# Kernel optimization log

Hardware: AMD Instinct MI355X
Metric: run time of the kernel (lower is better)

## Reference

```python
import jax, jax.numpy as jnp
import numpy as np
from jax import lax

B, S, E = 512, 128, 7
H = 1024
PRED_LEN = 96


def setup_inputs() -> dict:
    key = jax.random.key(0)
    ks = jax.random.split(key, 10)
    u = lambda k, shape: jax.random.uniform(k, shape, jnp.float32, -0.1, 0.1)
    return {
        "x": jax.random.normal(ks[0], (B, S, E), jnp.float32),
        "Wi0": u(ks[1], (4 * H, E)),
        "Wh0": u(ks[2], (4 * H, H)),
        "b0": u(ks[3], (4 * H,)),
        "Wi1": u(ks[4], (4 * H, H)),
        "Wh1": u(ks[5], (4 * H, H)),
        "b1": u(ks[6], (4 * H,)),
        "Wfc": u(ks[7], (PRED_LEN * E, H)),
        "bfc": u(ks[8], (PRED_LEN * E,)),
    }


def _lstm_layer(xs, Wi, Wh, b):
    # xs: [B, S, in] -> hs: [B, S, H]; gate order i, f, g, o
    batch = xs.shape[0]
    hidden = Wh.shape[1]
    # precompute input projections for all timesteps in one big GEMM
    x_proj = jnp.einsum("bsi,gi->bsg", xs, Wi) + b  # [B, S, 4H]

    def step(carry, xp_t):
        h, c = carry
        gates = xp_t + h @ Wh.T  # [B, 4H]
        i_t, f_t, g_t, o_t = jnp.split(gates, 4, axis=-1)
        i_t = jax.nn.sigmoid(i_t)
        f_t = jax.nn.sigmoid(f_t)
        g_t = jnp.tanh(g_t)
        o_t = jax.nn.sigmoid(o_t)
        c = f_t * c + i_t * g_t
        h = o_t * jnp.tanh(c)
        return (h, c), h

    h0 = jnp.zeros((batch, hidden), xs.dtype)
    c0 = jnp.zeros((batch, hidden), xs.dtype)
    (_, _), hs = lax.scan(step, (h0, c0), jnp.swapaxes(x_proj, 0, 1))
    return jnp.swapaxes(hs, 0, 1)  # [B, S, H]


def reference(x, Wi0, Wh0, b0, Wi1, Wh1, b1, Wfc, bfc):
    h1 = _lstm_layer(x, Wi0, Wh0, b0)
    h2 = _lstm_layer(h1, Wi1, Wh1, b1)
    last = h2[:, -1, :]  # [B, H]
    pred = last @ Wfc.T + bfc  # [B, PRED_LEN*E]
    return pred.reshape(x.shape[0], PRED_LEN, E)
```

## Files before the change

kernel.cpp:

```cpp
#include <hip/hip_runtime.h>
#include <hip/hip_bf16.h>


typedef __bf16 bf16x8 __attribute__((ext_vector_type(8)));
typedef float  f32x4  __attribute__((ext_vector_type(4)));

#define HSZ   (512 * 1024)

__device__ __forceinline__ float sigm_f(float x) {
    x = fminf(30.f, fmaxf(-30.f, x));
    return 1.0f / (1.0f + __expf(-x));
}
__device__ __forceinline__ float tanh_f(float x) {
    x = fminf(30.f, fmaxf(-30.f, x));
    float e = __expf(-2.0f * x);
    return (1.0f - e) / (1.0f + e);
}

__device__ __forceinline__ int perm_row(int np) {
    int g = (np >> 4) & 3;
    int j = ((np >> 6) << 4) | (np & 15);
    return g * 1024 + j;
}

__device__ __forceinline__ void spin_ge(const int* p, int target) {
    while (__hip_atomic_load(p, __ATOMIC_RELAXED, __HIP_MEMORY_SCOPE_AGENT) < target)
        __builtin_amdgcn_s_sleep(1);
}
__device__ __forceinline__ void signal_inc(int* p) {
    __hip_atomic_fetch_add(p, 1, __ATOMIC_RELAXED, __HIP_MEMORY_SCOPE_AGENT);
}
__device__ __forceinline__ void inv_l1() {
    asm volatile("buffer_inv" ::: "memory");
}
__device__ __forceinline__ void store_ea(unsigned* p, unsigned v) {
    __hip_atomic_store(p, v, __ATOMIC_RELAXED, __HIP_MEMORY_SCOPE_AGENT);
}


__global__ void prep_w0(const float* __restrict__ Wh0, __bf16* __restrict__ W0p) {
    int idx = blockIdx.x * 256 + threadIdx.x;
    int np = idx >> 8, k4 = (idx & 255) << 2;
    int r = perm_row(np);
    float4 v = *(const float4*)(Wh0 + r * 1024 + k4);
    __bf16* o = W0p + np * 1024 + k4;
    o[0] = (__bf16)v.x; o[1] = (__bf16)v.y; o[2] = (__bf16)v.z; o[3] = (__bf16)v.w;
}

__global__ void prep_w1(const float* __restrict__ Wi1, const float* __restrict__ Wh1,
                        __bf16* __restrict__ W1p) {
    int idx = blockIdx.x * 256 + threadIdx.x;
    int np = idx >> 9, k4 = (idx & 511) << 2;
    int r = perm_row(np);
    const float* s = (k4 < 1024) ? (Wi1 + r * 1024 + k4) : (Wh1 + r * 1024 + (k4 - 1024));
    float4 v = *(const float4*)s;
    __bf16* o = W1p + np * 2048 + k4;
    o[0] = (__bf16)v.x; o[1] = (__bf16)v.y; o[2] = (__bf16)v.z; o[3] = (__bf16)v.w;
}

__global__ void prep_wfc(const float* __restrict__ Wfc, __bf16* __restrict__ Wfcp) {
    int idx = blockIdx.x * 256 + threadIdx.x;
    int n = idx >> 8, k4 = (idx & 255) << 2;
    __bf16* o = Wfcp + n * 1024 + k4;
    if (n < 672) {
        float4 v = *(const float4*)(Wfc + n * 1024 + k4);
        o[0] = (__bf16)v.x; o[1] = (__bf16)v.y; o[2] = (__bf16)v.z; o[3] = (__bf16)v.w;
    } else {
        o[0] = (__bf16)0.f; o[1] = (__bf16)0.f; o[2] = (__bf16)0.f; o[3] = (__bf16)0.f;
    }
}

__global__ void prep_small(const float* __restrict__ Wi0, const float* __restrict__ b0,
                           const float* __restrict__ b1,
                           float* __restrict__ Wi0p, float* __restrict__ b1p) {
    int np = blockIdx.x * 256 + threadIdx.x;
    int r = perm_row(np);
    float* o = Wi0p + np * 8;
    #pragma unroll
    for (int q = 0; q < 7; ++q) o[q] = Wi0[r * 7 + q];
    o[7] = b0[r];
    b1p[np] = b1[r];
}


template <bool D0, bool D1>
__device__ __forceinline__ void floop(const __bf16* __restrict__ abase,
                                      const __bf16* __restrict__ w0row,
                                      const __bf16* __restrict__ w1row,
                                      int tid,
                                      char* AldsB, char* B0ldsB, char* B1ldsB,
                                      f32x4 (&acc0)[4], f32x4 (&acc1)[4]) {
    const int a_r = tid >> 3;
    const int a_c = (tid & 7) << 3;
    const int b_r = tid >> 2;
    const int b_c = (tid & 3) << 4;
    const int l  = tid & 63, w = tid >> 6;
    const int wm = w & 3,   wn = w >> 2;
    const int lj = l & 15,  lq = l >> 4;
    const int r7 = lj & 7;

    const __bf16* arw = abase + a_r * 1024 + a_c;

    const int awr  = a_r * 128 + (((tid & 7) ^ (a_r & 7)) << 4);
    const int bwr0 = b_r * 128 + (((((tid & 3) << 1) | 0) ^ (b_r & 7)) << 4);
    const int bwr1 = b_r * 128 + (((((tid & 3) << 1) | 1) ^ (b_r & 7)) << 4);
    const int rc0 = ((lq     ) ^ r7) << 4;
    const int rc1 = ((lq | 4 ) ^ r7) << 4;

    uint4 ra, rb00, rb01, rb10, rb11;
    auto ld = [&](int k0) {
        ra = *(const uint4*)(arw + k0);
        if (D0) {
            const __bf16* p = w0row + k0;
            rb00 = *(const uint4*)(p);
            rb01 = *(const uint4*)(p + 8);
        }
        if (D1) {
            const __bf16* p = w1row + k0;
            rb10 = *(const uint4*)(p);
            rb11 = *(const uint4*)(p + 8);
        }
    };
    auto wr = [&](int buf) {
        *(uint4*)(AldsB + buf * 8192 + awr) = ra;
        if (D0) {
            char* Bl = B0ldsB + buf * 16384;
            *(uint4*)(Bl + bwr0) = rb00;
            *(uint4*)(Bl + bwr1) = rb01;
        }
        if (D1) {
            char* Bl = B1ldsB + buf * 16384;
            *(uint4*)(Bl + bwr0) = rb10;
            *(uint4*)(Bl + bwr1) = rb11;
        }
    };

    ld(0);
    wr(0);
    ld(64);
    __syncthreads();

    const char* Ap  = AldsB  + (wm * 16 + lj) * 128;
    const char* B0p = B0ldsB + (wn * 64 + lj) * 128;
    const char* B1p = B1ldsB + (wn * 64 + lj) * 128;

    for (int it = 0; it < 16; ++it) {
        const int bo = it & 1;
        const char* Ab  = Ap  + bo * 8192;
        const char* B0b = B0p + bo * 16384;
        const char* B1b = B1p + bo * 16384;
        #pragma unroll
        for (int s = 0; s < 2; ++s) {
            const int rc = s ? rc1 : rc0;
            bf16x8 af = *(const bf16x8*)(Ab + rc);
            #pragma unroll
            for (int ni = 0; ni < 4; ++ni) {
                if (D0) {
                    bf16x8 b0 = *(const bf16x8*)(B0b + ni * 2048 + rc);
                    acc0[ni] = __builtin_amdgcn_mfma_f32_16x16x32_bf16(af, b0, acc0[ni], 0, 0, 0);
                }
                if (D1) {
                    bf16x8 b1 = *(const bf16x8*)(B1b + ni * 2048 + rc);
                    acc1[ni] = __builtin_amdgcn_mfma_f32_16x16x32_bf16(af, b1, acc1[ni], 0, 0, 0);
                }
            }
        }
        if (it + 1 < 16) wr((it + 1) & 1);
        if (it + 2 < 16) ld((it + 2) * 64);
        __syncthreads();
    }
}


__global__ __launch_bounds__(512)
void lstm_persist(const float* __restrict__ x,
                  const __bf16* __restrict__ W0p, const __bf16* __restrict__ W1p,
                  const __bf16* __restrict__ Wfcp,
                  const float* __restrict__ Wi0p, const float* __restrict__ b1p,
                  const float* __restrict__ bfc,
                  __bf16* __restrict__ bufA, __bf16* __restrict__ bufB,
                  char* __restrict__ flagpage, float* __restrict__ out) {
    __shared__ __attribute__((aligned(16))) char Alds[2 * 8192];
    __shared__ __attribute__((aligned(16))) char B0lds[2 * 16384];
    __shared__ __attribute__((aligned(16))) char B1lds[2 * 16384];
    __shared__ float Aux1[128];
    __shared__ float Xlds[64 * 9];
    __shared__ float Wxlds[128 * 9];
    __shared__ int role[2];

    const int tid = threadIdx.x;

    if (tid == 0) {
        int xcd = __builtin_amdgcn_s_getreg(63508) & 7;
        int* xcnt = (int*)(flagpage + 1024) + xcd;
        int slot = __hip_atomic_fetch_add(xcnt, 1, __ATOMIC_RELAXED,
                                          __HIP_MEMORY_SCOPE_AGENT);
        role[0] = xcd; role[1] = slot;
    }
    __syncthreads();
    const int xcd = role[0];
    const int sl  = role[1];
    const int mt = sl >> 2, nb = sl & 3;
    const int m0 = mt * 64;
    const int n0 = xcd * 512 + nb * 128;
    int* cnt = (int*)(flagpage + (size_t)mt * 64);

    if (tid < 128) {
        Aux1[tid] = b1p[n0 + tid];
    } else if (tid < 256) {
        int nl = tid - 128;
        const float* sp = Wi0p + (n0 + nl) * 8;
        float* d = Wxlds + nl * 9;
        #pragma unroll
        for (int q = 0; q < 8; ++q) d[q] = sp[q];
    }

    const int b_r = tid >> 2;
    const int b_c = (tid & 3) << 4;
    const int l  = tid & 63, w = tid >> 6;
    const int wm = w & 3,   wn = w >> 2;
    const int lj = l & 15,  lq = l >> 4;
    const int jc = (n0 >> 2) + wn * 16 + lj;

    const __bf16* w0row = W0p + (size_t)(n0 + b_r) * 1024 + b_c;
    const __bf16* w1row = W1p + (size_t)(n0 + b_r) * 2048 + b_c;

    float c0[4], c1[4];
    #pragma unroll
    for (int r = 0; r < 4; ++r) { c0[r] = 0.f; c1[r] = 0.f; }

    f32x4 acc0[4], acc1[4];

    for (int r = 0; r <= 128; ++r) {
        const bool do0 = (r < 128), do1 = (r > 0);
        const __bf16* haPrev = bufA + (size_t)(r % 3) * HSZ;
        __bf16*       haOut  = bufA + (size_t)((r + 1) % 3) * HSZ;
        const __bf16* hbPrev = bufB + (size_t)((r + 2) % 3) * HSZ;
        __bf16*       hbOut  = bufB + (size_t)(r % 3) * HSZ;

        if (tid == 0) spin_ge(cnt, 32 * r);
        __syncthreads();
        inv_l1();

        if (do0 && tid < 64) {
            const float* xr = x + (m0 + tid) * 896 + r * 7;
            float* d = Xlds + tid * 9;
            #pragma unroll
            for (int q = 0; q < 7; ++q) d[q] = xr[q];
            d[7] = 1.0f;
        }

        #pragma unroll
        for (int j = 0; j < 4; ++j) {
            acc0[j] = (f32x4){0.f, 0.f, 0.f, 0.f};
            acc1[j] = (f32x4){0.f, 0.f, 0.f, 0.f};
        }

        const __bf16* abase = haPrev + m0 * 1024;
        if (do0 && do1)
            floop<true, true >(abase, w0row, w1row, tid, Alds, B0lds, B1lds, acc0, acc1);
        else if (do0)
            floop<true, false>(abase, w0row, w1row, tid, Alds, B0lds, B1lds, acc0, acc1);
        else
            floop<false, true>(abase, w0row, w1row, tid, Alds, B0lds, B1lds, acc0, acc1);

        if (do1) {
            floop<false, true>(hbPrev + m0 * 1024, w0row, w1row + 1024,
                               tid, Alds, B0lds, B1lds, acc0, acc1);
        }

        if (do0) {
            #pragma unroll
            for (int rr = 0; rr < 4; ++rr) {
                int ml = wm * 16 + lq * 4 + rr;
                int m  = m0 + ml;
                float pre[4];
                #pragma unroll
                for (int g = 0; g < 4; ++g) pre[g] = acc0[g][rr];
                const float* xr = Xlds + ml * 9;
                #pragma unroll
                for (int g = 0; g < 4; ++g) {
                    const float* wx = Wxlds + (wn * 64 + g * 16 + lj) * 9;
                    float sv = 0.f;
                    #pragma unroll
                    for (int q = 0; q < 8; ++q) sv += xr[q] * wx[q];
                    pre[g] += sv;
                }
                float ig = sigm_f(pre[0]);
                float fg = sigm_f(pre[1]);
                float gv = tanh_f(pre[2]);
                float og = sigm_f(pre[3]);
                float cn = fg * c0[rr] + ig * gv;
                c0[rr] = cn;
                float hv = og * tanh_f(cn);
                unsigned u32 = __builtin_bit_cast(unsigned, hv);
                unsigned hu = (u32 + 0x7fffu + ((u32 >> 16) & 1u)) >> 16;
                int pv = __shfl_xor((int)hu, 1, 64);
                if ((lj & 1) == 0)
                    store_ea((unsigned*)(haOut + (size_t)m * 1024 + jc),
                             hu | ((unsigned)pv << 16));
            }
        }
        if (do1) {
            #pragma unroll
            for (int rr = 0; rr < 4; ++rr) {
                int m = m0 + wm * 16 + lq * 4 + rr;
                float pre[4];
                #pragma unroll
                for (int g = 0; g < 4; ++g)
                    pre[g] = acc1[g][rr] + Aux1[wn * 64 + g * 16 + lj];
                float ig = sigm_f(pre[0]);
                float fg = sigm_f(pre[1]);
                float gv = tanh_f(pre[2]);
                float og = sigm_f(pre[3]);
                float cn = fg * c1[rr] + ig * gv;
                c1[rr] = cn;
                float hv = og * tanh_f(cn);
                unsigned u32 = __builtin_bit_cast(unsigned, hv);
                unsigned hu = (u32 + 0x7fffu + ((u32 >> 16) & 1u)) >> 16;
                int pv = __shfl_xor((int)hu, 1, 64);
                if ((lj & 1) == 0)
                    store_ea((unsigned*)(hbOut + (size_t)m * 1024 + jc),
                             hu | ((unsigned)pv << 16));
            }
        }
        __syncthreads();
        if (tid == 0) signal_inc(cnt);
    }

    if (nb == 0 && xcd < 6) {
        const int n0fc = xcd * 128;
        if (tid == 0) spin_ge(cnt, 32 * 129);
        __syncthreads();
        inv_l1();
        if (tid < 128) {
            int n = n0fc + tid;
            Aux1[tid] = (n < 672) ? bfc[n] : 0.f;
        }
        #pragma unroll
        for (int j = 0; j < 4; ++j)
            acc0[j] = (f32x4){0.f, 0.f, 0.f, 0.f};
        floop<true, false>(bufB + (size_t)2 * HSZ + m0 * 1024,
                           Wfcp + (size_t)(n0fc + b_r) * 1024 + b_c, nullptr,
                           tid, Alds, B0lds, B1lds, acc0, acc1);
        #pragma unroll
        for (int rr = 0; rr < 4; ++rr) {
            int m = m0 + wm * 16 + lq * 4 + rr;
            #pragma unroll
            for (int ni = 0; ni < 4; ++ni) {
                int n = n0fc + wn * 64 + ni * 16 + lj;
                if (n < 672)
                    out[m * 672 + n] = acc0[ni][rr] + Aux1[wn * 64 + ni * 16 + lj];
            }
        }
    }
}

#define O_W0P   0u
#define O_W1P   8388608u
#define O_WFCP  25165824u
#define O_WI0P  26738688u
#define O_B1P   26869760u
#define O_FLG   26886144u
#define O_BA    26888192u
#define O_BB    30033920u
#define WS_NEED 33179648u

extern "C" void kernel_launch(void* const* d_in, const int* in_sizes, int n_in,
                              void* d_out, int out_size, void* d_ws, size_t ws_size,
                              hipStream_t stream) {
    const float* x   = (const float*)d_in[0];
    const float* Wi0 = (const float*)d_in[1];
    const float* Wh0 = (const float*)d_in[2];
    const float* b0  = (const float*)d_in[3];
    const float* Wi1 = (const float*)d_in[4];
    const float* Wh1 = (const float*)d_in[5];
    const float* b1  = (const float*)d_in[6];
    const float* Wfc = (const float*)d_in[7];
    const float* bfc = (const float*)d_in[8];
    float* out = (float*)d_out;
    char*  ws  = (char*)d_ws;
    if (ws_size < WS_NEED) return;

    __bf16* W0p  = (__bf16*)(ws + O_W0P);
    __bf16* W1p  = (__bf16*)(ws + O_W1P);
    __bf16* Wfcp = (__bf16*)(ws + O_WFCP);
    float*  Wi0p = (float*)(ws + O_WI0P);
    float*  b1p  = (float*)(ws + O_B1P);
    char*   flg  = (char*)(ws + O_FLG);
    __bf16* bufA = (__bf16*)(ws + O_BA);
    __bf16* bufB = (__bf16*)(ws + O_BB);

    hipMemsetAsync(ws + O_FLG, 0, 2048u + 1048576u, stream);
    hipMemsetAsync(ws + O_BB, 0, 1048576u, stream);

    prep_w0   <<<4096, 256, 0, stream>>>(Wh0, W0p);
    prep_w1   <<<8192, 256, 0, stream>>>(Wi1, Wh1, W1p);
    prep_wfc  <<<768,  256, 0, stream>>>(Wfc, Wfcp);
    prep_small<<<16,   256, 0, stream>>>(Wi0, b0, b1, Wi0p, b1p);

    lstm_persist<<<256, 512, 0, stream>>>(x, W0p, W1p, Wfcp, Wi0p, b1p, bfc,
                                          bufA, bufB, flg, out);
}
```

Before: 2.925 ms.

## Retile recurrent GEMM to 2x2 warp tiles with LDS-staged coalesced h stores

Changes the per-warp MFMA tiling from 16x64 to a 32x32 (2x2 of 16x16) layout, so each A and B fragment read from LDS feeds two MFMAs. The gate permutation is regrouped into blocks of 8 so each lane computes two gate activations, exchanged with lane shuffles instead of four sigmoid/tanh calls. The inner loop gets a three-stage register prefetch with explicit waitcnt/barrier syncs. Hidden-state outputs are staged in LDS and written back with coalesced 32-bit stores rather than scattered strided stores. The cost is extra shuffles, an additional barrier per step, and a more intricate schedule.

Measured after the change: 2.956 ms. Within noise of the previous version (+1.1%).

```diff
diff --git a/kernel.cpp b/kernel.cpp
--- a/kernel.cpp
+++ b/kernel.cpp
@@ -7,10 +7,6 @@
 
 #define HSZ   (512 * 1024)
 
-__device__ __forceinline__ float sigm_f(float x) {
-    x = fminf(30.f, fmaxf(-30.f, x));
-    return 1.0f / (1.0f + __expf(-x));
-}
 __device__ __forceinline__ float tanh_f(float x) {
     x = fminf(30.f, fmaxf(-30.f, x));
     float e = __expf(-2.0f * x);
@@ -18,8 +14,8 @@
 }
 
 __device__ __forceinline__ int perm_row(int np) {
-    int g = (np >> 4) & 3;
-    int j = ((np >> 6) << 4) | (np & 15);
+    int g = (np >> 3) & 3;
+    int j = ((np >> 5) << 3) | (np & 7);
     return g * 1024 + j;
 }
 
@@ -89,13 +85,12 @@
                                       const __bf16* __restrict__ w1row,
                                       int tid,
                                       char* AldsB, char* B0ldsB, char* B1ldsB,
-                                      f32x4 (&acc0)[4], f32x4 (&acc1)[4]) {
+                                      f32x4 (&acc0)[2][2], f32x4 (&acc1)[2][2]) {
     const int a_r = tid >> 3;
     const int a_c = (tid & 7) << 3;
     const int b_r = tid >> 2;
-    const int b_c = (tid & 3) << 4;
     const int l  = tid & 63, w = tid >> 6;
-    const int wm = w & 3,   wn = w >> 2;
+    const int wm2 = w >> 2, wn4 = w & 3;
     const int lj = l & 15,  lq = l >> 4;
     const int r7 = lj & 7;
 
@@ -104,71 +99,82 @@
     const int awr  = a_r * 128 + (((tid & 7) ^ (a_r & 7)) << 4);
     const int bwr0 = b_r * 128 + (((((tid & 3) << 1) | 0) ^ (b_r & 7)) << 4);
     const int bwr1 = b_r * 128 + (((((tid & 3) << 1) | 1) ^ (b_r & 7)) << 4);
-    const int rc0 = ((lq     ) ^ r7) << 4;
-    const int rc1 = ((lq | 4 ) ^ r7) << 4;
-
-    uint4 ra, rb00, rb01, rb10, rb11;
-    auto ld = [&](int k0) {
-        ra = *(const uint4*)(arw + k0);
-        if (D0) {
-            const __bf16* p = w0row + k0;
-            rb00 = *(const uint4*)(p);
-            rb01 = *(const uint4*)(p + 8);
-        }
-        if (D1) {
-            const __bf16* p = w1row + k0;
-            rb10 = *(const uint4*)(p);
-            rb11 = *(const uint4*)(p + 8);
-        }
-    };
-    auto wr = [&](int buf) {
-        *(uint4*)(AldsB + buf * 8192 + awr) = ra;
-        if (D0) {
-            char* Bl = B0ldsB + buf * 16384;
-            *(uint4*)(Bl + bwr0) = rb00;
-            *(uint4*)(Bl + bwr1) = rb01;
-        }
-        if (D1) {
-            char* Bl = B1ldsB + buf * 16384;
-            *(uint4*)(Bl + bwr0) = rb10;
-            *(uint4*)(Bl + bwr1) = rb11;
-        }
-    };
-
-    ld(0);
-    wr(0);
-    ld(64);
-    __syncthreads();
-
-    const char* Ap  = AldsB  + (wm * 16 + lj) * 128;
-    const char* B0p = B0ldsB + (wn * 64 + lj) * 128;
-    const char* B1p = B1ldsB + (wn * 64 + lj) * 128;
-
-    for (int it = 0; it < 16; ++it) {
-        const int bo = it & 1;
-        const char* Ab  = Ap  + bo * 8192;
-        const char* B0b = B0p + bo * 16384;
-        const char* B1b = B1p + bo * 16384;
-        #pragma unroll
-        for (int s = 0; s < 2; ++s) {
-            const int rc = s ? rc1 : rc0;
-            bf16x8 af = *(const bf16x8*)(Ab + rc);
-            #pragma unroll
-            for (int ni = 0; ni < 4; ++ni) {
-                if (D0) {
-                    bf16x8 b0 = *(const bf16x8*)(B0b + ni * 2048 + rc);
-                    acc0[ni] = __builtin_amdgcn_mfma_f32_16x16x32_bf16(af, b0, acc0[ni], 0, 0, 0);
-                }
-                if (D1) {
-                    bf16x8 b1 = *(const bf16x8*)(B1b + ni * 2048 + rc);
-                    acc1[ni] = __builtin_amdgcn_mfma_f32_16x16x32_bf16(af, b1, acc1[ni], 0, 0, 0);
-                }
-            }
-        }
-        if (it + 1 < 16) wr((it + 1) & 1);
-        if (it + 2 < 16) ld((it + 2) * 64);
-        __syncthreads();
-    }
+    const int rc0 = ((lq    ) ^ r7) << 4;
+    const int rc1 = ((lq | 4) ^ r7) << 4;
+
+    const char* ArowA  = AldsB  + (wm2 * 32      + lj) * 128;
+    const char* ArowB  = AldsB  + (wm2 * 32 + 16 + lj) * 128;
+    const char* B0rowA = B0ldsB + (wn4 * 32      + lj) * 128;
+    const char* B0rowB = B0ldsB + (wn4 * 32 + 16 + lj) * 128;
+    const char* B1rowA = B1ldsB + (wn4 * 32      + lj) * 128;
+    const char* B1rowB = B1ldsB + (wn4 * 32 + 16 + lj) * 128;
+
+    uint4 vA0, vP0, vP1, vQ0, vQ1;
+    uint4 vA1, vR0, vR1, vS0, vS1;
+
+#define FL_LD(Av, P0v, P1v, Q0v, Q1v, k0) do {                                 \
+    Av = *(const uint4*)(arw + (k0));                                          \
+    if (D0) { P0v = *(const uint4*)(w0row + (k0));                             \
+              P1v = *(const uint4*)(w0row + (k0) + 8); }                       \
+    if (D1) { Q0v = *(const uint4*)(w1row + (k0));                             \
+              Q1v = *(const uint4*)(w1row + (k0) + 8); } } while (0)
+
+#define FL_WR(Av, P0v, P1v, Q0v, Q1v, buf) do {                                \
+    *(uint4*)(AldsB + (buf) * 8192 + awr) = Av;                                \
+    if (D0) { *(uint4*)(B0ldsB + (buf) * 16384 + bwr0) = P0v;                  \
+              *(uint4*)(B0ldsB + (buf) * 16384 + bwr1) = P1v; }                \
+    if (D1) { *(uint4*)(B1ldsB + (buf) * 16384 + bwr0) = Q0v;                  \
+              *(uint4*)(B1ldsB + (buf) * 16384 + bwr1) = Q1v; } } while (0)
+
+#define FL_MM(bo) do {                                                         \
+    _Pragma("unroll")                                                          \
+    for (int s = 0; s < 2; ++s) {                                              \
+        const int rc = s ? rc1 : rc0;                                          \
+        bf16x8 af0 = *(const bf16x8*)(ArowA + (bo) * 8192 + rc);               \
+        bf16x8 af1 = *(const bf16x8*)(ArowB + (bo) * 8192 + rc);               \
+        if (D0) {                                                              \
+            bf16x8 b00 = *(const bf16x8*)(B0rowA + (bo) * 16384 + rc);         \
+            bf16x8 b01 = *(const bf16x8*)(B0rowB + (bo) * 16384 + rc);         \
+            acc0[0][0] = __builtin_amdgcn_mfma_f32_16x16x32_bf16(af0, b00, acc0[0][0], 0, 0, 0); \
+            acc0[1][0] = __builtin_amdgcn_mfma_f32_16x16x32_bf16(af1, b00, acc0[1][0], 0, 0, 0); \
+            acc0[0][1] = __builtin_amdgcn_mfma_f32_16x16x32_bf16(af0, b01, acc0[0][1], 0, 0, 0); \
+            acc0[1][1] = __builtin_amdgcn_mfma_f32_16x16x32_bf16(af1, b01, acc0[1][1], 0, 0, 0); \
+        }                                                                      \
+        if (D1) {                                                              \
+            bf16x8 b10 = *(const bf16x8*)(B1rowA + (bo) * 16384 + rc);         \
+            bf16x8 b11 = *(const bf16x8*)(B1rowB + (bo) * 16384 + rc);         \
+            acc1[0][0] = __builtin_amdgcn_mfma_f32_16x16x32_bf16(af0, b10, acc1[0][0], 0, 0, 0); \
+            acc1[1][0] = __builtin_amdgcn_mfma_f32_16x16x32_bf16(af1, b10, acc1[1][0], 0, 0, 0); \
+            acc1[0][1] = __builtin_amdgcn_mfma_f32_16x16x32_bf16(af0, b11, acc1[0][1], 0, 0, 0); \
+            acc1[1][1] = __builtin_amdgcn_mfma_f32_16x16x32_bf16(af1, b11, acc1[1][1], 0, 0, 0); \
+        }                                                                      \
+    } } while (0)
+
+#define FL_SYNC() do {                                                         \
+    asm volatile("s_waitcnt lgkmcnt(0)" ::: "memory");                         \
+    __builtin_amdgcn_s_barrier();                                              \
+    __builtin_amdgcn_sched_barrier(0); } while (0)
+
+    FL_LD(vA0, vP0, vP1, vQ0, vQ1, 0);
+    FL_WR(vA0, vP0, vP1, vQ0, vQ1, 0);
+    FL_LD(vA1, vR0, vR1, vS0, vS1, 64);
+    FL_LD(vA0, vP0, vP1, vQ0, vQ1, 128);
+    FL_SYNC();
+
+    for (int t = 0; t < 8; ++t) {
+        FL_MM(0);
+        FL_WR(vA1, vR0, vR1, vS0, vS1, 1);
+        if (2 * t + 3 < 16) FL_LD(vA1, vR0, vR1, vS0, vS1, (2 * t + 3) * 64);
+        FL_SYNC();
+        FL_MM(1);
+        if (2 * t + 2 < 16) FL_WR(vA0, vP0, vP1, vQ0, vQ1, 0);
+        if (2 * t + 4 < 16) FL_LD(vA0, vP0, vP1, vQ0, vQ1, (2 * t + 4) * 64);
+        FL_SYNC();
+    }
+#undef FL_LD
+#undef FL_WR
+#undef FL_MM
+#undef FL_SYNC
 }
 
 
@@ -183,6 +189,7 @@
     __shared__ __attribute__((aligned(16))) char Alds[2 * 8192];
     __shared__ __attribute__((aligned(16))) char B0lds[2 * 16384];
     __shared__ __attribute__((aligned(16))) char B1lds[2 * 16384];
+    __shared__ unsigned Hs[2][64 * 16];
     __shared__ float Aux1[128];
     __shared__ float Xlds[64 * 9];
     __shared__ float Wxlds[128 * 9];
@@ -214,22 +221,38 @@
         #pragma unroll
         for (int q = 0; q < 8; ++q) d[q] = sp[q];
     }
+    __syncthreads();
 
     const int b_r = tid >> 2;
     const int b_c = (tid & 3) << 4;
     const int l  = tid & 63, w = tid >> 6;
-    const int wm = w & 3,   wn = w >> 2;
+    const int wm2 = w >> 2, wn4 = w & 3;
     const int lj = l & 15,  lq = l >> 4;
-    const int jc = (n0 >> 2) + wn * 16 + lj;
+    const int lh = lj >> 3;
+    const int cg0 = wn4 * 32 + lj;
+    const int cg1 = wn4 * 32 + 16 + lj;
+    const float g2_1 = (lh == 0) ? 1.f : 0.f;
+    const float sc1 = 1.f + g2_1;
+
+    const float b1v0 = Aux1[cg0];
+    const float b1v1 = Aux1[cg1];
+    float wx0r[8], wx1r[8];
+    #pragma unroll
+    for (int q = 0; q < 8; ++q) {
+        wx0r[q] = Wxlds[cg0 * 9 + q];
+        wx1r[q] = Wxlds[cg1 * 9 + q];
+    }
 
     const __bf16* w0row = W0p + (size_t)(n0 + b_r) * 1024 + b_c;
     const __bf16* w1row = W1p + (size_t)(n0 + b_r) * 2048 + b_c;
 
-    float c0[4], c1[4];
+    float c0s[2][4], c1s[2][4];
     #pragma unroll
-    for (int r = 0; r < 4; ++r) { c0[r] = 0.f; c1[r] = 0.f; }
-
-    f32x4 acc0[4], acc1[4];
+    for (int i = 0; i < 2; ++i)
+        #pragma unroll
+        for (int j = 0; j < 4; ++j) { c0s[i][j] = 0.f; c1s[i][j] = 0.f; }
+
+    f32x4 acc0[2][2], acc1[2][2];
 
     for (int r = 0; r <= 128; ++r) {
         const bool do0 = (r < 128), do1 = (r > 0);
@@ -251,10 +274,12 @@
         }
 
         #pragma unroll
-        for (int j = 0; j < 4; ++j) {
-            acc0[j] = (f32x4){0.f, 0.f, 0.f, 0.f};
-            acc1[j] = (f32x4){0.f, 0.f, 0.f, 0.f};
-        }
+        for (int i = 0; i < 2; ++i)
+            #pragma unroll
+            for (int j = 0; j < 2; ++j) {
+                acc0[i][j] = (f32x4){0.f, 0.f, 0.f, 0.f};
+                acc1[i][j] = (f32x4){0.f, 0.f, 0.f, 0.f};
+            }
 
         const __bf16* abase = haPrev + m0 * 1024;
         if (do0 && do1)
@@ -271,57 +296,82 @@
 
         if (do0) {
             #pragma unroll
-            for (int rr = 0; rr < 4; ++rr) {
-                int ml = wm * 16 + lq * 4 + rr;
-                int m  = m0 + ml;
-                float pre[4];
+            for (int mi = 0; mi < 2; ++mi) {
                 #pragma unroll
-                for (int g = 0; g < 4; ++g) pre[g] = acc0[g][rr];
-                const float* xr = Xlds + ml * 9;
+                for (int rr = 0; rr < 4; ++rr) {
+                    int row = wm2 * 32 + mi * 16 + lq * 4 + rr;
+                    const float* xr = Xlds + row * 9;
+                    float pre0 = acc0[mi][0][rr];
+                    float pre1 = acc0[mi][1][rr];
+                    #pragma unroll
+                    for (int q = 0; q < 8; ++q) {
+                        pre0 += xr[q] * wx0r[q];
+                        pre1 += xr[q] * wx1r[q];
+                    }
+                    float px0 = fminf(30.f, fmaxf(-30.f, pre0));
+                    float e0  = __expf(-px0);
+                    float a0  = 1.f / (1.f + e0);
+                    float px1 = fminf(30.f, fmaxf(-30.f, pre1 * sc1));
+                    float e1  = __expf(-px1);
+                    float a1  = (1.f - g2_1 * e1) / (1.f + e1);
+                    float p0 = __shfl_xor(a0, 8, 64);
+                    float p1 = __shfl_xor(a1, 8, 64);
+                    float ig = lh ? p0 : a0;
+                    float fg = lh ? a0 : p0;
+                    float gv = lh ? p1 : a1;
+                    float og = lh ? a1 : p1;
+                    float cn = fg * c0s[mi][rr] + ig * gv;
+                    c0s[mi][rr] = cn;
+                    float hv = og * tanh_f(cn);
+                    unsigned u32 = __builtin_bit_cast(unsigned, hv);
+                    unsigned hu = (u32 + 0x7fffu + ((u32 >> 16) & 1u)) >> 16;
+                    int pv = __shfl_xor((int)hu, 1, 64);
+                    if (lh == 0 && (lj & 1) == 0)
+                        Hs[0][row * 16 + wn4 * 4 + (lj >> 1)] = hu | ((unsigned)pv << 16);
+                }
+            }
+        }
+        if (do1) {
+            #pragma unroll
+            for (int mi = 0; mi < 2; ++mi) {
                 #pragma unroll
-                for (int g = 0; g < 4; ++g) {
-                    const float* wx = Wxlds + (wn * 64 + g * 16 + lj) * 9;
-                    float sv = 0.f;
-                    #pragma unroll
-                    for (int q = 0; q < 8; ++q) sv += xr[q] * wx[q];
-                    pre[g] += sv;
+                for (int rr = 0; rr < 4; ++rr) {
+                    int row = wm2 * 32 + mi * 16 + lq * 4 + rr;
+                    float pre0 = acc1[mi][0][rr] + b1v0;
+                    float pre1 = acc1[mi][1][rr] + b1v1;
+                    float px0 = fminf(30.f, fmaxf(-30.f, pre0));
+                    float e0  = __expf(-px0);
+                    float a0  = 1.f / (1.f + e0);
+                    float px1 = fminf(30.f, fmaxf(-30.f, pre1 * sc1));
+                    float e1  = __expf(-px1);
+                    float a1  = (1.f - g2_1 * e1) / (1.f + e1);
+                    float p0 = __shfl_xor(a0, 8, 64);
+                    float p1 = __shfl_xor(a1, 8, 64);
+                    float ig = lh ? p0 : a0;
+                    float fg = lh ? a0 : p0;
+                    float gv = lh ? p1 : a1;
+                    float og = lh ? a1 : p1;
+                    float cn = fg * c1s[mi][rr] + ig * gv;
+                    c1s[mi][rr] = cn;
+                    float hv = og * tanh_f(cn);
+                    unsigned u32 = __builtin_bit_cast(unsigned, hv);
+                    unsigned hu = (u32 + 0x7fffu + ((u32 >> 16) & 1u)) >> 16;
+                    int pv = __shfl_xor((int)hu, 1, 64);
+                    if (lh == 0 && (lj & 1) == 0)
+                        Hs[1][row * 16 + wn4 * 4 + (lj >> 1)] = hu | ((unsigned)pv << 16);
                 }
-                float ig = sigm_f(pre[0]);
-                float fg = sigm_f(pre[1]);
-                float gv = tanh_f(pre[2]);
-                float og = sigm_f(pre[3]);
-                float cn = fg * c0[rr] + ig * gv;
-                c0[rr] = cn;
-                float hv = og * tanh_f(cn);
-                unsigned u32 = __builtin_bit_cast(unsigned, hv);
-                unsigned hu = (u32 + 0x7fffu + ((u32 >> 16) & 1u)) >> 16;
-                int pv = __shfl_xor((int)hu, 1, 64);
-                if ((lj & 1) == 0)
-                    store_ea((unsigned*)(haOut + (size_t)m * 1024 + jc),
-                             hu | ((unsigned)pv << 16));
             }
         }
-        if (do1) {
-            #pragma unroll
-            for (int rr = 0; rr < 4; ++rr) {
-                int m = m0 + wm * 16 + lq * 4 + rr;
-                float pre[4];
-                #pragma unroll
-                for (int g = 0; g < 4; ++g)
-                    pre[g] = acc1[g][rr] + Aux1[wn * 64 + g * 16 + lj];
-                float ig = sigm_f(pre[0]);
-                float fg = sigm_f(pre[1]);
-                float gv = tanh_f(pre[2]);
-                float og = sigm_f(pre[3]);
-                float cn = fg * c1[rr] + ig * gv;
-                c1[rr] = cn;
-                float hv = og * tanh_f(cn);
-                unsigned u32 = __builtin_bit_cast(unsigned, hv);
-                unsigned hu = (u32 + 0x7fffu + ((u32 >> 16) & 1u)) >> 16;
-                int pv = __shfl_xor((int)hu, 1, 64);
-                if ((lj & 1) == 0)
-                    store_ea((unsigned*)(hbOut + (size_t)m * 1024 + jc),
-                             hu | ((unsigned)pv << 16));
+        __syncthreads();
+
+        {
+            #pragma unroll
+            for (int pass = 0; pass < 2; ++pass) {
+                int d = pass * 512 + tid;
+                int row = d >> 4, col = d & 15;
+                size_t off = (size_t)(m0 + row) * 512 + (n0 >> 3) + col;
+                if (do0) store_ea((unsigned*)haOut + off, Hs[0][d]);
+                if (do1) store_ea((unsigned*)hbOut + off, Hs[1][d]);
             }
         }
         __syncthreads();
@@ -338,19 +388,24 @@
             Aux1[tid] = (n < 672) ? bfc[n] : 0.f;
         }
         #pragma unroll
-        for (int j = 0; j < 4; ++j)
-            acc0[j] = (f32x4){0.f, 0.f, 0.f, 0.f};
+        for (int i = 0; i < 2; ++i)
+            #pragma unroll
+            for (int j = 0; j < 2; ++j)
+                acc0[i][j] = (f32x4){0.f, 0.f, 0.f, 0.f};
         floop<true, false>(bufB + (size_t)2 * HSZ + m0 * 1024,
                            Wfcp + (size_t)(n0fc + b_r) * 1024 + b_c, nullptr,
                            tid, Alds, B0lds, B1lds, acc0, acc1);
+        const float bv0 = Aux1[cg0];
+        const float bv1 = Aux1[cg1];
         #pragma unroll
-        for (int rr = 0; rr < 4; ++rr) {
-            int m = m0 + wm * 16 + lq * 4 + rr;
-            #pragma unroll
-            for (int ni = 0; ni < 4; ++ni) {
-                int n = n0fc + wn * 64 + ni * 16 + lj;
-                if (n < 672)
-                    out[m * 672 + n] = acc0[ni][rr] + Aux1[wn * 64 + ni * 16 + lj];
+        for (int mi = 0; mi < 2; ++mi) {
+            #pragma unroll
+            for (int rr = 0; rr < 4; ++rr) {
+                int m = m0 + wm2 * 32 + mi * 16 + lq * 4 + rr;
+                int nA = n0fc + cg0;
+                int nB = n0fc + cg1;
+                if (nA < 672) out[m * 672 + nA] = acc0[mi][0][rr] + bv0;
+                if (nB < 672) out[m * 672 + nB] = acc0[mi][1][rr] + bv1;
             }
         }
     }
```
